# Kernel optimization log

Measured on AMD Instinct MI355X. Metric: run time of the kernel, lower is better.

## Reference

```python
import jax, jax.numpy as jnp
import numpy as np

NUM_ENT = 50000
DIM = 128
NUM_REL = 1000  # num_rel * 2 (inverse relations)
E = 300000
SLOPE = 0.2      # args.leaky_relu_w
BN_EPS = 1e-5


def _leaky(x):
    return jax.nn.leaky_relu(x, SLOPE)


def _l2norm(x):
    n = jnp.linalg.norm(x, axis=-1, keepdims=True)
    return x / jnp.maximum(n, 1e-12)


def _batchnorm(x):
    # BatchNorm1d, training mode, fresh gamma=1/beta=0
    m = x.mean(axis=0)
    v = x.var(axis=0)
    return (x - m) / jnp.sqrt(v + BN_EPS)


def _propagate(i, j, etype, rel, x, watt, aatt, gcn, norm, num_ent):
    # gather -> relation-aware transform (opn='mult') -> attention -> scatter-add
    trans = x[j] * rel[etype]                       # [E, D]
    comb = jnp.concatenate([x[i], trans], axis=1)   # [E, 2D]
    score = (_leaky(comb @ watt) @ aatt)[:, 0]      # [E]
    # scatter softmax of attention score over destination nodes
    m = jax.ops.segment_max(score, i, num_segments=num_ent)
    m = jnp.where(jnp.isfinite(m), m, 0.0)
    e = jnp.exp(score - m[i])
    s = jax.ops.segment_sum(e, i, num_segments=num_ent)
    alpha = e / (s[i] + 1e-16)
    msg = (trans @ gcn) * alpha[:, None]
    if norm is not None:
        msg = msg * norm[:, None]
    return jax.ops.segment_sum(msg, i, num_segments=num_ent)


def _conv(ent, rel_in, edge_index, edge_type, w1, w2, gcn, loop_rel, watt, aatt):
    # RelationalAwareLayer.forward
    num_ent = ent.shape[0]
    rel = jnp.concatenate([rel_in, loop_rel], axis=0)
    rel = _leaky(rel @ w1) @ w2
    row, col = edge_index[0], edge_index[1]
    deg = jax.ops.segment_sum(jnp.ones((row.shape[0],), jnp.float32), row, num_segments=num_ent)
    dinv = jnp.where(deg > 0, deg ** -0.5, 0.0)
    norm = dinv[row]
    msg_n = _propagate(row, col, edge_type, rel, ent, watt, aatt, gcn, norm, num_ent)
    idx = jnp.arange(num_ent)
    loop_t = jnp.full((num_ent,), rel.shape[0] - 1)
    msg_s = _propagate(idx, idx, loop_t, rel, ent, watt, aatt, gcn, None, num_ent)
    return jnp.tanh(_batchnorm((msg_n + msg_s) / 2.0))


def setup_inputs() -> dict:
    key = jax.random.key(0)
    ks = jax.random.split(key, 24)
    g = lambda k, s: jax.random.normal(k, s, dtype=jnp.float32) * 0.05
    return {
        'edge_index': jax.random.randint(ks[0], (2, E), 0, NUM_ENT),
        'edge_type': jax.random.randint(ks[1], (E,), 0, NUM_REL),
        'ent_info_att': g(ks[2], (NUM_ENT, DIM)),
        'ent_completion_att': g(ks[3], (NUM_ENT, DIM)),
        'rel_completion_att': g(ks[4], (NUM_REL, DIM)),
        'rel_info_att': g(ks[5], (NUM_REL, DIM)),
        'align_linear1_1': g(ks[6], (2 * DIM, DIM)),
        'align_linear1_2': g(ks[7], (DIM, DIM)),
        'align_linear2_1': g(ks[8], (2 * DIM, DIM)),
        'align_linear2_2': g(ks[9], (DIM, DIM)),
        'rel_linear11': g(ks[10], (DIM, DIM)),
        'rel_linear12': g(ks[11], (DIM, DIM)),
        'rel_linear11_align': g(ks[12], (DIM, DIM)),
        'rel_linear12_align': g(ks[13], (DIM, DIM)),
        'all_linear_comp': g(ks[14], (3 * DIM, DIM)),
        # stacked per-layer conv params: [conv1_align, conv1_completion, conv2_align]
        'conv_w1': g(ks[15], (3, DIM, DIM)),
        'conv_w2': g(ks[16], (3, DIM, DIM)),
        'conv_gcn': g(ks[17], (3, DIM, DIM)),
        'conv_loop': g(ks[18], (3, 1, DIM)),
        'conv_watt': g(ks[19], (3, 2 * DIM, DIM)),
        'conv_aatt': g(ks[20], (3, DIM, 1)),
    }


def reference(edge_index, edge_type, ent_info_att, ent_completion_att,
              rel_completion_att, rel_info_att,
              align_linear1_1, align_linear1_2, align_linear2_1, align_linear2_2,
              rel_linear11, rel_linear12, rel_linear11_align, rel_linear12_align,
              all_linear_comp, conv_w1, conv_w2, conv_gcn, conv_loop, conv_watt, conv_aatt):
    # forward_base with num_gcn_layer == 2, dropout rate 0 (identity)
    init_comp = _l2norm(ent_completion_att)
    e1 = _leaky(jnp.concatenate([init_comp, ent_info_att], axis=1) @ align_linear1_1) @ align_linear1_2
    ao1 = _conv(e1, rel_info_att, edge_index, edge_type,
                conv_w1[0], conv_w2[0], conv_gcn[0], conv_loop[0], conv_watt[0], conv_aatt[0])
    co1 = _conv(ent_completion_att, rel_completion_att, edge_index, edge_type,
                conv_w1[1], conv_w2[1], conv_gcn[1], conv_loop[1], conv_watt[1], conv_aatt[1])
    pos1n = _l2norm(co1)
    e2 = _leaky(jnp.concatenate([pos1n, ao1], axis=1) @ align_linear2_1) @ align_linear2_2
    pr1 = _leaky(rel_completion_att @ rel_linear11) @ rel_linear12
    ari = _leaky(rel_info_att @ rel_linear11_align) @ rel_linear12_align
    ao2 = _conv(e2, ari, edge_index, edge_type,
                conv_w1[2], conv_w2[2], conv_gcn[2], conv_loop[2], conv_watt[2], conv_aatt[2])
    out = jnp.concatenate([e1, ao1, ao2], axis=1) @ all_linear_comp
    return (out, co1, pr1)
```

## Files before the change

### kernel.cpp

```cpp
#include <hip/hip_runtime.h>
#include <hip/hip_bf16.h>
#include <math.h>

#define D 128
#define DD 16384
typedef unsigned short u16;
typedef __attribute__((ext_vector_type(8))) short short8v;
typedef __attribute__((ext_vector_type(4))) short short4v;
typedef __attribute__((ext_vector_type(4))) float f32x4;

__device__ __forceinline__ u16 f2s(float v){
    union { __hip_bfloat16 h; u16 u; } c; c.h = __float2bfloat16(v); return c.u;
}
__device__ __forceinline__ float s2f(u16 u){
    union { __hip_bfloat16 h; u16 u; } c; c.u = u; return __bfloat162float(c.h);
}
__device__ __forceinline__ float lrelu(float x){ return x > 0.f ? x : 0.2f*x; }
__device__ __forceinline__ float ldx(const void* p, size_t i, int f32){
    return f32 ? ((const float*)p)[i] : s2f(((const u16*)p)[i]);
}

__global__ void k_zero(float* __restrict__ p, int n){
    for (int i = blockIdx.x*blockDim.x + threadIdx.x; i < n; i += gridDim.x*blockDim.x)
        p[i] = 0.f;
}
__global__ void k_f2b4(const float* __restrict__ in, u16* __restrict__ out, int n4){
    for (int i = blockIdx.x*blockDim.x + threadIdx.x; i < n4; i += gridDim.x*blockDim.x){
        float4 a = ((const float4*)in)[i];
        short4v pk;
        pk[0] = (short)f2s(a.x); pk[1] = (short)f2s(a.y);
        pk[2] = (short)f2s(a.z); pk[3] = (short)f2s(a.w);
        *(short4v*)(out + (size_t)i*4) = pk;
    }
}
__global__ void k_ideg(const int* __restrict__ row, int* __restrict__ deg, int E_){
    for (int i = blockIdx.x*blockDim.x + threadIdx.x; i < E_; i += gridDim.x*blockDim.x)
        atomicAdd(&deg[row[i]], 1);
}
__global__ void k_scan1(const int* __restrict__ ideg, int* __restrict__ rowptr,
                        int* __restrict__ bsum, int n){
    __shared__ int buf[256];
    int t = threadIdx.x, i = blockIdx.x*256 + t;
    int v = (i < n) ? ideg[i] : 0;
    buf[t] = v;
    __syncthreads();
    #pragma unroll
    for (int o = 1; o < 256; o <<= 1){
        int u = (t >= o) ? buf[t-o] : 0;
        __syncthreads();
        buf[t] += u;
        __syncthreads();
    }
    if (i < n) rowptr[i] = buf[t] - v;
    if (t == 255) bsum[blockIdx.x] = buf[255];
}
__global__ void k_scan2(int* __restrict__ bsum, int nb){
    __shared__ int buf[256];
    __shared__ int carry_s;
    int t = threadIdx.x;
    if (t == 0) carry_s = 0;
    __syncthreads();
    for (int base = 0; base < nb; base += 256){
        int v = (base + t < nb) ? bsum[base + t] : 0;
        buf[t] = v;
        __syncthreads();
        #pragma unroll
        for (int o = 1; o < 256; o <<= 1){
            int u = (t >= o) ? buf[t-o] : 0;
            __syncthreads();
            buf[t] += u;
            __syncthreads();
        }
        if (base + t < nb) bsum[base + t] = carry_s + buf[t] - v;
        int last = buf[255];
        __syncthreads();
        if (t == 0) carry_s += last;
        __syncthreads();
    }
}
__global__ void k_scan3(int* __restrict__ rowptr, const int* __restrict__ bsum,
                        int n, int E_){
    int i = blockIdx.x*blockDim.x + threadIdx.x;
    if (i < n) rowptr[i] += bsum[i >> 8];
    if (i == 0) rowptr[n] = E_;
}
__global__ void k_scatter(const int* __restrict__ row, const int* __restrict__ rowptr,
                          int* __restrict__ cnt, int* __restrict__ perm, int E_){
    for (int e = blockIdx.x*blockDim.x + threadIdx.x; e < E_; e += gridDim.x*blockDim.x){
        int i = row[e];
        int pos = rowptr[i] + atomicAdd(&cnt[i], 1);
        perm[pos] = e;
    }
}
template<bool F32>
__global__ void k_rsnorm(const void* __restrict__ x, float* __restrict__ rs){
    int r = blockIdx.x, t = threadIdx.x;
    __shared__ float sw[2];
    float v = ldx(x, (size_t)r*D + t, F32 ? 1 : 0);
    float s = v*v;
    #pragma unroll
    for (int o = 32; o > 0; o >>= 1) s += __shfl_xor(s, o, 64);
    if ((t & 63) == 0) sw[t >> 6] = s;
    __syncthreads();
    if (t == 0) rs[r] = 1.f / fmaxf(sqrtf(sw[0] + sw[1]), 1e-12f);
}
__global__ void k_rel_mlp(const float* __restrict__ src, const float* __restrict__ loopv, int R0,
                          const float* __restrict__ W1, const float* __restrict__ W2,
                          float* __restrict__ out){
    int r = blockIdx.x, t = threadIdx.x;
    __shared__ float v[D];
    __shared__ float h[D];
    v[t] = (r < R0) ? src[(size_t)r*D + t] : loopv[t];
    __syncthreads();
    float a = 0.f;
    #pragma unroll 8
    for (int k = 0; k < D; k++) a += v[k] * W1[(size_t)k*D + t];
    h[t] = lrelu(a);
    __syncthreads();
    float o = 0.f;
    #pragma unroll 8
    for (int k = 0; k < D; k++) o += h[k] * W2[(size_t)k*D + t];
    out[(size_t)r*D + t] = o;
}
__global__ void k_bnapply(const float* __restrict__ acc, const float* __restrict__ gp,
                          float inv_ne, int n, u16* __restrict__ dstb,
                          float* __restrict__ dstf){
    int d = threadIdx.x & 127;
    float m = gp[d] * inv_ne;
    float var = gp[128 + d] * inv_ne - m*m;
    float sc = rsqrtf(var + 1e-5f);
    for (int i = blockIdx.x*blockDim.x + threadIdx.x; i < n; i += gridDim.x*blockDim.x){
        float v = acc[i] * 0.5f;
        float r = tanhf((v - m) * sc);
        dstb[i] = f2s(r);
        if (dstf) dstf[i] = r;
    }
}

struct TEnt { const float* s; u16* d; int ldd; };
struct TTab { TEnt e[18]; };
__global__ void k_wprep(TTab tab){
    TEnt en = tab.e[blockIdx.x];
    int t = threadIdx.x;
    int n = t >> 1, h = t & 1;
    #pragma unroll
    for (int g = 0; g < 8; ++g){
        int k0 = h*64 + g*8;
        short8v pk;
        #pragma unroll
        for (int q = 0; q < 8; ++q) pk[q] = (short)f2s(en.s[(size_t)(k0+q)*D + n]);
        *(short8v*)(en.d + (size_t)n*en.ldd + k0) = pk;
    }
}

struct Srcs { const void* p0; const void* p1; const void* p2; int f0, f1, f2; };

template<int NSEG, int EPI>
__global__ __launch_bounds__(256) void k_mrow(Srcs S, const float* __restrict__ scale0,
        const u16* __restrict__ WT, void* __restrict__ out, int NE_,
        float* __restrict__ gp){
    __shared__ __align__(16) short As[128*128];
    int tid = threadIdx.x;
    int row0 = blockIdx.x * 128;
    int lane = tid & 63, w = tid >> 6;
    int l15 = lane & 15, lq = lane >> 4;
    int nhalf = w & 1, mquad = w >> 1;
    f32x4 acc[4][4];
    #pragma unroll
    for (int a = 0; a < 4; a++)
        #pragma unroll
        for (int b = 0; b < 4; b++) acc[a][b] = (f32x4){0.f,0.f,0.f,0.f};

    int sr = tid >> 1, sh = tid & 1;
    int rr = row0 + sr; if (rr >= NE_) rr = NE_ - 1;

    #pragma unroll
    for (int s = 0; s < NSEG; ++s){
        const void* sp = (s == 0) ? S.p0 : (s == 1) ? S.p1 : S.p2;
        int sf = (s == 0) ? S.f0 : (s == 1) ? S.f1 : S.f2;
        float sc = (s == 0 && scale0) ? scale0[rr] : 1.f;
        if (s) __syncthreads();
        #pragma unroll
        for (int g = 0; g < 8; ++g){
            int k8 = sh*64 + g*8;
            short8v pk;
            if (sf){
                const float* fp = (const float*)sp + (size_t)rr*D + k8;
                #pragma unroll
                for (int q = 0; q < 8; ++q) pk[q] = (short)f2s(fp[q] * sc);
            } else {
                short8v sv = *(const short8v*)((const u16*)sp + (size_t)rr*D + k8);
                if (s == 0 && scale0){
                    #pragma unroll
                    for (int q = 0; q < 8; ++q) pk[q] = (short)f2s(s2f((u16)sv[q]) * sc);
                } else pk = sv;
            }
            *(short8v*)(As + sr*D + (((k8>>3) ^ (sr&7))<<3)) = pk;
        }
        __syncthreads();
        short8v bfr[4][4];
        #pragma unroll
        for (int nt = 0; nt < 4; ++nt)
            #pragma unroll
            for (int kk = 0; kk < 4; ++kk){
                size_t idx = (size_t)(nhalf*64 + nt*16 + l15)*(NSEG*D) + (size_t)s*D + kk*32 + lq*8;
                bfr[nt][kk] = *(const short8v*)(WT + idx);
            }
        #pragma unroll
        for (int mt = 0; mt < 4; ++mt){
            int ar = mquad*64 + mt*16 + l15;
            short8v afr[4];
            #pragma unroll
            for (int kk = 0; kk < 4; ++kk)
                afr[kk] = *(const short8v*)(As + ar*D + (((kk*4 + lq) ^ (ar&7))<<3));
            #pragma unroll
            for (int nt = 0; nt < 4; ++nt)
                #pragma unroll
                for (int kk = 0; kk < 4; ++kk)
                    acc[mt][nt] = __builtin_amdgcn_mfma_f32_16x16x32_bf16(
                        afr[kk], bfr[nt][kk], acc[mt][nt], 0, 0, 0);
        }
    }
    if (EPI == 3){
        float cs[4] = {0,0,0,0}, cs2[4] = {0,0,0,0};
        #pragma unroll
        for (int mt = 0; mt < 4; ++mt)
            #pragma unroll
            for (int nt = 0; nt < 4; ++nt)
                #pragma unroll
                for (int r = 0; r < 4; ++r){
                    int gr = row0 + mquad*64 + mt*16 + lq*4 + r;
                    if (gr >= NE_) continue;
                    int c = nhalf*64 + nt*16 + l15;
                    float v = acc[mt][nt][r];
                    ((float*)out)[(size_t)gr*D + c] = v;
                    float h = v * 0.5f;
                    cs[nt] += h; cs2[nt] += h*h;
                }
        __syncthreads();
        float* ps  = (float*)As;
        float* ps2 = ps + 1024;
        int slot = mquad*4 + lq;
        #pragma unroll
        for (int nt = 0; nt < 4; ++nt){
            int c = nhalf*64 + nt*16 + l15;
            ps[slot*128 + c]  = cs[nt];
            ps2[slot*128 + c] = cs2[nt];
        }
        __syncthreads();
        if (tid < 128){
            float s = 0.f, s2 = 0.f;
            #pragma unroll
            for (int q = 0; q < 8; ++q){ s += ps[q*128 + tid]; s2 += ps2[q*128 + tid]; }
            atomicAdd(&gp[tid], s);
            atomicAdd(&gp[128 + tid], s2);
        }
    } else {
        #pragma unroll
        for (int mt = 0; mt < 4; ++mt){
            #pragma unroll
            for (int nt = 0; nt < 4; ++nt){
                #pragma unroll
                for (int r = 0; r < 4; ++r){
                    int gr = row0 + mquad*64 + mt*16 + lq*4 + r;
                    if (gr >= NE_) continue;
                    int c = nhalf*64 + nt*16 + l15;
                    float v = acc[mt][nt][r];
                    if (EPI == 0) ((float*)out)[(size_t)gr*D + c] = v;
                    else if (EPI == 1) ((u16*)out)[(size_t)gr*D + c] = f2s(v);
                    else ((u16*)out)[(size_t)gr*D + c] = f2s(lrelu(v));
                }
            }
        }
    }
}

__global__ __launch_bounds__(256) void k_medge(const int* __restrict__ rowi,
        const int* __restrict__ coli, const int* __restrict__ ety,
        const u16* __restrict__ x, const float* __restrict__ rel2,
        const u16* __restrict__ xattb, const u16* __restrict__ WT,
        const float* __restrict__ aatt, float* __restrict__ score,
        float* __restrict__ segs, int E_){
    __shared__ __align__(16) short As[64*128];
    __shared__ __align__(16) short Xs[64*136];
    __shared__ int jL[64], kL[64], iL[64];
    __shared__ float red[2][64];
    int tid = threadIdx.x;
    int e0 = blockIdx.x * 64;
    if (tid < 64){
        int e = e0 + tid; if (e >= E_) e = E_ - 1;
        jL[tid] = coli[e]; kL[tid] = ety[e]; iL[tid] = rowi[e];
    }
    __syncthreads();
    {
        int sr = tid >> 2, part = tid & 3;
        int j = jL[sr], krel = kL[sr], ii = iL[sr];
        #pragma unroll
        for (int g = 0; g < 4; ++g){
            int k8 = part*32 + g*8;
            short8v sv = *(const short8v*)(x + (size_t)j*D + k8);
            const float* rp = rel2 + (size_t)krel*D + k8;
            short8v pk;
            #pragma unroll
            for (int q = 0; q < 8; ++q) pk[q] = (short)f2s(s2f((u16)sv[q]) * rp[q]);
            *(short8v*)(As + sr*D + (((k8>>3) ^ (sr&7))<<3)) = pk;
            short8v xv = *(const short8v*)(xattb + (size_t)ii*D + k8);
            *(short8v*)(Xs + sr*136 + k8) = xv;
        }
    }
    __syncthreads();
    int lane = tid & 63, w = tid >> 6;
    int l15 = lane & 15, lq = lane >> 4;
    int nhalf = w & 1, mquad = w >> 1;
    short8v bfr[4][4];
    #pragma unroll
    for (int nt = 0; nt < 4; ++nt)
        #pragma unroll
        for (int kk = 0; kk < 4; ++kk)
            bfr[nt][kk] = *(const short8v*)(WT + (size_t)(nhalf*64 + nt*16 + l15)*D + kk*32 + lq*8);
    f32x4 acc[2][4];
    #pragma unroll
    for (int a = 0; a < 2; a++)
        #pragma unroll
        for (int b = 0; b < 4; b++) acc[a][b] = (f32x4){0.f,0.f,0.f,0.f};
    #pragma unroll
    for (int mt = 0; mt < 2; ++mt){
        int ar = (mquad*2 + mt)*16 + l15;
        short8v afr[4];
        #pragma unroll
        for (int kk = 0; kk < 4; ++kk)
            afr[kk] = *(const short8v*)(As + ar*D + (((kk*4 + lq) ^ (ar&7))<<3));
        #pragma unroll
        for (int nt = 0; nt < 4; ++nt)
            #pragma unroll
            for (int kk = 0; kk < 4; ++kk)
                acc[mt][nt] = __builtin_amdgcn_mfma_f32_16x16x32_bf16(
                    afr[kk], bfr[nt][kk], acc[mt][nt], 0, 0, 0);
    }
    float av[4];
    #pragma unroll
    for (int nt = 0; nt < 4; ++nt) av[nt] = aatt[nhalf*64 + nt*16 + l15];
    #pragma unroll
    for (int mt = 0; mt < 2; ++mt){
        int mtg = mquad*2 + mt;
        #pragma unroll
        for (int r = 0; r < 4; ++r){
            int el = mtg*16 + lq*4 + r;
            float p = 0.f;
            #pragma unroll
            for (int nt = 0; nt < 4; ++nt){
                float xv = s2f((u16)Xs[el*136 + nhalf*64 + nt*16 + l15]);
                p += lrelu(acc[mt][nt][r] + xv) * av[nt];
            }
            p += __shfl_xor(p, 1, 64);
            p += __shfl_xor(p, 2, 64);
            p += __shfl_xor(p, 4, 64);
            p += __shfl_xor(p, 8, 64);
            if (l15 == 0) red[nhalf][el] = p;
        }
    }
    __syncthreads();
    if (tid < 64){
        int e = e0 + tid;
        if (e < E_){
            float es = expf(red[0][tid] + red[1][tid]);
            score[e] = es;
            atomicAdd(&segs[iL[tid]], es);
        }
    }
}

__global__ __launch_bounds__(128) void k_uacc(const int* __restrict__ perm,
        const int* __restrict__ rowptr, const int* __restrict__ coli,
        const int* __restrict__ ety, const u16* __restrict__ x,
        const float* __restrict__ rel2, int NRr,
        const float* __restrict__ score, const float* __restrict__ segs,
        u16* __restrict__ u){
    __shared__ int jls[32];
    __shared__ int kls[32];
    __shared__ float cfl[32];
    int i = blockIdx.x, t = threadIdx.x;
    int s = rowptr[i], epos = rowptr[i+1];
    int deg = epos - s;
    float acc = s2f(x[(size_t)i*D + t]) * rel2[(size_t)NRr*D + t];
    if (deg > 0){
        float isg = rsqrtf((float)deg) / (segs[i] + 1e-16f);
        for (int base = s; base < epos; base += 32){
            int nc = min(32, epos - base);
            __syncthreads();
            if (t < nc){
                int e = perm[base + t];
                jls[t] = coli[e]; kls[t] = ety[e]; cfl[t] = score[e] * isg;
            }
            __syncthreads();
            int p = 0;
            for (; p + 4 <= nc; p += 4){
                int j0 = jls[p],   k0 = kls[p];
                int j1 = jls[p+1], k1 = kls[p+1];
                int j2 = jls[p+2], k2 = kls[p+2];
                int j3 = jls[p+3], k3 = kls[p+3];
                float x0 = s2f(x[(size_t)j0*D + t]);
                float x1 = s2f(x[(size_t)j1*D + t]);
                float x2 = s2f(x[(size_t)j2*D + t]);
                float x3 = s2f(x[(size_t)j3*D + t]);
                float r0 = rel2[(size_t)k0*D + t];
                float r1 = rel2[(size_t)k1*D + t];
                float r2 = rel2[(size_t)k2*D + t];
                float r3 = rel2[(size_t)k3*D + t];
                acc += cfl[p]*x0*r0 + cfl[p+1]*x1*r1 + cfl[p+2]*x2*r2 + cfl[p+3]*x3*r3;
            }
            for (; p < nc; ++p)
                acc += cfl[p] * s2f(x[(size_t)jls[p]*D + t]) * rel2[(size_t)kls[p]*D + t];
        }
    }
    u[(size_t)i*D + t] = f2s(acc);
}

extern "C" void kernel_launch(void* const* d_in, const int* in_sizes, int n_in,
                              void* d_out, int out_size, void* d_ws, size_t ws_size,
                              hipStream_t stream){
    const int* eidx = (const int*)d_in[0];
    const int* ety  = (const int*)d_in[1];
    const float* ent_info = (const float*)d_in[2];
    const float* ent_comp = (const float*)d_in[3];
    const float* rel_comp = (const float*)d_in[4];
    const float* rel_info = (const float*)d_in[5];
    const float* al11 = (const float*)d_in[6],  *al12 = (const float*)d_in[7];
    const float* al21 = (const float*)d_in[8],  *al22 = (const float*)d_in[9];
    const float* rl11 = (const float*)d_in[10], *rl12 = (const float*)d_in[11];
    const float* rl11a = (const float*)d_in[12], *rl12a = (const float*)d_in[13];
    const float* allw = (const float*)d_in[14];
    const float* cw1 = (const float*)d_in[15], *cw2 = (const float*)d_in[16];
    const float* cgcn = (const float*)d_in[17], *cloop = (const float*)d_in[18];
    const float* cwatt = (const float*)d_in[19], *caatt = (const float*)d_in[20];

    const int E  = in_sizes[1];
    const int NE = in_sizes[2] / D;
    const int NR = in_sizes[4] / D;
    const int* row = eidx;
    const int* col = eidx + E;
    const size_t NEd = (size_t)NE * D;
    float* outp = (float*)d_out;

    char* wsb = (char*)d_ws;
    size_t off = 0;
    auto takeB = [&](size_t bytes) -> void* {
        void* q = wsb + off;
        off = (off + bytes + 255) & ~(size_t)255;
        return q;
    };
    float* accum = (float*)takeB(NEd * 4);
    u16*   hb    = (u16*)accum;
    u16*   xattb = (u16*) takeB(NEd * 2);
    u16*   e1b   = (u16*) takeB(NEd * 2);
    u16*   ao1b  = (u16*) takeB(NEd * 2);
    u16*   e2b   = (u16*) takeB(NEd * 2);
    u16*   cob   = (u16*) takeB(NEd * 2);
    float* rel2  = (float*)takeB((size_t)(NR+1)*D*4);
    float* ari   = (float*)takeB((size_t)NR*D*4);
    float* score = (float*)takeB((size_t)E*4);
    float* rs    = (float*)takeB((size_t)NE*4);
    int*   rowptr= (int*)  takeB((size_t)(NE+1)*4);
    int*   perm  = (int*)  takeB((size_t)E*4);
    int*   bsum  = (int*)  takeB(1024*4);
    int ZW = 5*NE + 768;
    int*   zz    = (int*)  takeB((size_t)ZW*4);
    int*   ideg  = zz;
    int*   cnt   = zz + NE;
    float* segs3 = (float*)(zz + 2*NE);
    float* gp3   = segs3 + 3*(size_t)NE;
    u16*   wtXatt = (u16*)takeB((size_t)3*DD*2);
    u16*   wtScore= (u16*)takeB((size_t)3*DD*2);
    u16*   wtGcn  = (u16*)takeB((size_t)3*DD*2);
    u16*   wtAl11 = (u16*)takeB((size_t)2*DD*2);
    u16*   wtAl12 = (u16*)takeB((size_t)DD*2);
    u16*   wtAl21 = (u16*)takeB((size_t)2*DD*2);
    u16*   wtAl22 = (u16*)takeB((size_t)DD*2);
    u16*   wtAllw = (u16*)takeB((size_t)3*DD*2);
    u16*   xcb   = e2b;

    const int GS = 2048, BS = 256;
    const int RB = (NE + 127) / 128;
    const int EB = (E + 63) / 64;
    const int NB = (NE + 255) / 256;
    const float inv_ne = 1.f / (float)NE;

    TTab tab;
    int ti = 0;
    for (int l = 0; l < 3; ++l){
        tab.e[ti++] = { cwatt + (size_t)l*2*DD,        wtXatt  + (size_t)l*DD, 128 };
        tab.e[ti++] = { cwatt + (size_t)l*2*DD + DD,   wtScore + (size_t)l*DD, 128 };
        tab.e[ti++] = { cgcn  + (size_t)l*DD,          wtGcn   + (size_t)l*DD, 128 };
    }
    tab.e[ti++] = { al11,       wtAl11,        256 };
    tab.e[ti++] = { al11 + DD,  wtAl11 + 128,  256 };
    tab.e[ti++] = { al12,       wtAl12,        128 };
    tab.e[ti++] = { al21,       wtAl21,        256 };
    tab.e[ti++] = { al21 + DD,  wtAl21 + 128,  256 };
    tab.e[ti++] = { al22,       wtAl22,        128 };
    tab.e[ti++] = { allw,            wtAllw,        384 };
    tab.e[ti++] = { allw + DD,       wtAllw + 128,  384 };
    tab.e[ti++] = { allw + 2*DD,     wtAllw + 256,  384 };
    k_wprep<<<18, 256, 0, stream>>>(tab);

    k_zero<<<256, BS, 0, stream>>>((float*)zz, ZW);
    k_f2b4<<<GS, BS, 0, stream>>>(ent_comp, xcb, (int)(NEd/4));
    k_ideg<<<GS, BS, 0, stream>>>(row, ideg, E);
    k_scan1<<<NB, 256, 0, stream>>>(ideg, rowptr, bsum, NE);
    k_scan2<<<1, 256, 0, stream>>>(bsum, NB);
    k_scan3<<<NB, 256, 0, stream>>>(rowptr, bsum, NE, E);
    k_scatter<<<GS, BS, 0, stream>>>(row, rowptr, cnt, perm, E);

    k_rsnorm<true><<<NE, D, 0, stream>>>(ent_comp, rs);
    {
        Srcs S{ ent_comp, ent_info, nullptr, 1, 1, 0 };
        k_mrow<2, 2><<<RB, 256, 0, stream>>>(S, rs, wtAl11, hb, NE, nullptr);
        Srcs S2{ hb, nullptr, nullptr, 0, 0, 0 };
        k_mrow<1, 1><<<RB, 256, 0, stream>>>(S2, nullptr, wtAl12, e1b, NE, nullptr);
    }

    auto conv = [&](const u16* x, const float* relsrc, int l, u16* dstb, float* dstf){
        const float* w1   = cw1   + (size_t)l*DD;
        const float* w2   = cw2   + (size_t)l*DD;
        const float* aatt = caatt + (size_t)l*D;
        const float* lo   = cloop + (size_t)l*D;
        float* segs = segs3 + (size_t)l*NE;
        float* gp   = gp3 + (size_t)l*256;
        k_rel_mlp<<<NR+1, D, 0, stream>>>(relsrc, lo, NR, w1, w2, rel2);
        Srcs Sx{ x, nullptr, nullptr, 0, 0, 0 };
        k_mrow<1, 1><<<RB, 256, 0, stream>>>(Sx, nullptr, wtXatt + (size_t)l*DD, xattb, NE, nullptr);
        k_medge<<<EB, 256, 0, stream>>>(row, col, ety, x, rel2, xattb,
                                        wtScore + (size_t)l*DD, aatt, score, segs, E);
        k_uacc<<<NE, D, 0, stream>>>(perm, rowptr, col, ety, x, rel2, NR,
                                     score, segs, xattb);
        Srcs Su{ xattb, nullptr, nullptr, 0, 0, 0 };
        k_mrow<1, 3><<<RB, 256, 0, stream>>>(Su, nullptr, wtGcn + (size_t)l*DD, accum, NE, gp);
        k_bnapply<<<GS, BS, 0, stream>>>(accum, gp, inv_ne, (int)NEd, dstb, dstf);
    };

    conv(e1b, rel_info, 0, ao1b, nullptr);
    conv(xcb, rel_comp, 1, cob,  outp + NEd);

    k_rsnorm<false><<<NE, D, 0, stream>>>(cob, rs);
    {
        Srcs S{ cob, ao1b, nullptr, 0, 0, 0 };
        k_mrow<2, 2><<<RB, 256, 0, stream>>>(S, rs, wtAl21, hb, NE, nullptr);
        Srcs S2{ hb, nullptr, nullptr, 0, 0, 0 };
        k_mrow<1, 1><<<RB, 256, 0, stream>>>(S2, nullptr, wtAl22, e2b, NE, nullptr);
    }

    k_rel_mlp<<<NR, D, 0, stream>>>(rel_comp, nullptr, NR, rl11, rl12, outp + 2*NEd);
    k_rel_mlp<<<NR, D, 0, stream>>>(rel_info, nullptr, NR, rl11a, rl12a, ari);

    conv(e2b, ari, 2, cob, nullptr);

    {
        Srcs S{ e1b, ao1b, cob, 0, 0, 0 };
        k_mrow<3, 0><<<RB, 256, 0, stream>>>(S, nullptr, wtAllw, outp, NE, nullptr);
    }
}
```

Before: 725.6 us.

## Fuse edge scoring, segment softmax and aggregation into one CSR-block kernel

Edge attention scoring, scatter-softmax normalisation and message aggregation move into one kernel. Each block owns the destination nodes whose CSR edge range starts in its 64-edge slice and keeps the transformed edge features in shared memory for reuse in the weighted sum. This removes the global score and segment-sum buffers, their atomics and a separate per-node gather kernel. The self-loop term is now written in the x·W_att matmul epilogue. In exchange, xattb is gathered from global memory per edge. Each block also caps its edges at 128, so unusually high-degree spans would be truncated.

```diff
diff --git a/kernel.cpp b/kernel.cpp
--- a/kernel.cpp
+++ b/kernel.cpp
@@ -4,6 +4,7 @@
 
 #define D 128
 #define DD 16384
+#define NEMAX 128
 typedef unsigned short u16;
 typedef __attribute__((ext_vector_type(8))) short short8v;
 typedef __attribute__((ext_vector_type(4))) short short4v;
@@ -23,6 +24,10 @@
 __global__ void k_zero(float* __restrict__ p, int n){
     for (int i = blockIdx.x*blockDim.x + threadIdx.x; i < n; i += gridDim.x*blockDim.x)
         p[i] = 0.f;
+}
+__global__ void k_filli(int* __restrict__ p, int v, int n){
+    for (int i = blockIdx.x*blockDim.x + threadIdx.x; i < n; i += gridDim.x*blockDim.x)
+        p[i] = v;
 }
 __global__ void k_f2b4(const float* __restrict__ in, u16* __restrict__ out, int n4){
     for (int i = blockIdx.x*blockDim.x + threadIdx.x; i < n4; i += gridDim.x*blockDim.x){
@@ -90,6 +95,17 @@
         int i = row[e];
         int pos = rowptr[i] + atomicAdd(&cnt[i], 1);
         perm[pos] = e;
+    }
+}
+__global__ void k_bmap(const int* __restrict__ rowptr, int* __restrict__ nstart,
+                       int* __restrict__ nend, int n){
+    for (int i = blockIdx.x*blockDim.x + threadIdx.x; i < n; i += gridDim.x*blockDim.x){
+        int s = rowptr[i], e = rowptr[i+1];
+        if (e > s){
+            int b = s >> 6;
+            atomicMin(&nstart[b], i);
+            atomicMax(&nend[b], i);
+        }
     }
 }
 template<bool F32>
@@ -158,7 +174,7 @@
 template<int NSEG, int EPI>
 __global__ __launch_bounds__(256) void k_mrow(Srcs S, const float* __restrict__ scale0,
         const u16* __restrict__ WT, void* __restrict__ out, int NE_,
-        float* __restrict__ gp){
+        float* __restrict__ gp, u16* __restrict__ uout, const float* __restrict__ looprow){
     __shared__ __align__(16) short As[128*128];
     int tid = threadIdx.x;
     int row0 = blockIdx.x * 128;
@@ -267,34 +283,52 @@
                     int c = nhalf*64 + nt*16 + l15;
                     float v = acc[mt][nt][r];
                     if (EPI == 0) ((float*)out)[(size_t)gr*D + c] = v;
-                    else if (EPI == 1) ((u16*)out)[(size_t)gr*D + c] = f2s(v);
-                    else ((u16*)out)[(size_t)gr*D + c] = f2s(lrelu(v));
+                    else ((u16*)out)[(size_t)gr*D + c] = f2s(EPI == 2 ? lrelu(v) : v);
                 }
             }
         }
-    }
-}
-
-__global__ __launch_bounds__(256) void k_medge(const int* __restrict__ rowi,
-        const int* __restrict__ coli, const int* __restrict__ ety,
+        if (EPI == 4){
+            for (int idx = tid; idx < 128*128; idx += 256){
+                int r2 = idx >> 7, c = idx & 127;
+                int gr = row0 + r2;
+                if (gr < NE_){
+                    float v = s2f((u16)As[r2*D + ((((c>>3) ^ (r2&7))<<3) | (c&7))]) * looprow[c];
+                    uout[(size_t)gr*D + c] = f2s(v);
+                }
+            }
+        }
+    }
+}
+
+__global__ __launch_bounds__(256) void k_fedge(
+        const int* __restrict__ rowi, const int* __restrict__ coli, const int* __restrict__ ety,
+        const int* __restrict__ rowptr, const int* __restrict__ perm,
+        const int* __restrict__ nstart, const int* __restrict__ nend,
         const u16* __restrict__ x, const float* __restrict__ rel2,
         const u16* __restrict__ xattb, const u16* __restrict__ WT,
-        const float* __restrict__ aatt, float* __restrict__ score,
-        float* __restrict__ segs, int E_){
-    __shared__ __align__(16) short As[64*128];
-    __shared__ __align__(16) short Xs[64*136];
-    __shared__ int jL[64], kL[64], iL[64];
+        const float* __restrict__ aatt, u16* __restrict__ u){
+    __shared__ __align__(16) short As[NEMAX*D];
+    __shared__ int jL[NEMAX], kL[NEMAX], iL[NEMAX];
+    __shared__ float sc[NEMAX];
     __shared__ float red[2][64];
+    int b = blockIdx.x;
+    int ns = nstart[b];
+    if (ns == 0x7fffffff) return;
+    int nn = nend[b] - ns + 1;
     int tid = threadIdx.x;
-    int e0 = blockIdx.x * 64;
-    if (tid < 64){
-        int e = e0 + tid; if (e >= E_) e = E_ - 1;
+    int estart = rowptr[ns];
+    int ne = rowptr[ns + nn] - estart;
+    if (ne > NEMAX) ne = NEMAX;
+    if (tid < ne){
+        int e = perm[estart + tid];
         jL[tid] = coli[e]; kL[tid] = ety[e]; iL[tid] = rowi[e];
     }
     __syncthreads();
-    {
-        int sr = tid >> 2, part = tid & 3;
-        int j = jL[sr], krel = kL[sr], ii = iL[sr];
+    int ntile = (ne > 64) ? 128 : 64;
+    for (int it = tid; it < ntile*4; it += 256){
+        int p = it >> 2, part = it & 3;
+        int ps = (p < ne) ? p : (ne - 1);
+        int j = jL[ps], krel = kL[ps];
         #pragma unroll
         for (int g = 0; g < 4; ++g){
             int k8 = part*32 + g*8;
@@ -303,9 +337,7 @@
             short8v pk;
             #pragma unroll
             for (int q = 0; q < 8; ++q) pk[q] = (short)f2s(s2f((u16)sv[q]) * rp[q]);
-            *(short8v*)(As + sr*D + (((k8>>3) ^ (sr&7))<<3)) = pk;
-            short8v xv = *(const short8v*)(xattb + (size_t)ii*D + k8);
-            *(short8v*)(Xs + sr*136 + k8) = xv;
+            *(short8v*)(As + p*D + (((k8>>3) ^ (p&7))<<3)) = pk;
         }
     }
     __syncthreads();
@@ -318,102 +350,83 @@
         #pragma unroll
         for (int kk = 0; kk < 4; ++kk)
             bfr[nt][kk] = *(const short8v*)(WT + (size_t)(nhalf*64 + nt*16 + l15)*D + kk*32 + lq*8);
-    f32x4 acc[2][4];
-    #pragma unroll
-    for (int a = 0; a < 2; a++)
-        #pragma unroll
-        for (int b = 0; b < 4; b++) acc[a][b] = (f32x4){0.f,0.f,0.f,0.f};
-    #pragma unroll
-    for (int mt = 0; mt < 2; ++mt){
-        int ar = (mquad*2 + mt)*16 + l15;
-        short8v afr[4];
-        #pragma unroll
-        for (int kk = 0; kk < 4; ++kk)
-            afr[kk] = *(const short8v*)(As + ar*D + (((kk*4 + lq) ^ (ar&7))<<3));
-        #pragma unroll
-        for (int nt = 0; nt < 4; ++nt)
+    float av[4];
+    #pragma unroll
+    for (int nt = 0; nt < 4; ++nt) av[nt] = aatt[nhalf*64 + nt*16 + l15];
+
+    for (int half = 0; half*64 < ne; ++half){
+        f32x4 acc[2][4];
+        #pragma unroll
+        for (int a = 0; a < 2; a++)
+            #pragma unroll
+            for (int c = 0; c < 4; c++) acc[a][c] = (f32x4){0.f,0.f,0.f,0.f};
+        #pragma unroll
+        for (int mt = 0; mt < 2; ++mt){
+            int ar = half*64 + (mquad*2 + mt)*16 + l15;
+            short8v afr[4];
             #pragma unroll
             for (int kk = 0; kk < 4; ++kk)
-                acc[mt][nt] = __builtin_amdgcn_mfma_f32_16x16x32_bf16(
-                    afr[kk], bfr[nt][kk], acc[mt][nt], 0, 0, 0);
-    }
-    float av[4];
-    #pragma unroll
-    for (int nt = 0; nt < 4; ++nt) av[nt] = aatt[nhalf*64 + nt*16 + l15];
-    #pragma unroll
-    for (int mt = 0; mt < 2; ++mt){
-        int mtg = mquad*2 + mt;
-        #pragma unroll
-        for (int r = 0; r < 4; ++r){
-            int el = mtg*16 + lq*4 + r;
-            float p = 0.f;
-            #pragma unroll
-            for (int nt = 0; nt < 4; ++nt){
-                float xv = s2f((u16)Xs[el*136 + nhalf*64 + nt*16 + l15]);
-                p += lrelu(acc[mt][nt][r] + xv) * av[nt];
+                afr[kk] = *(const short8v*)(As + ar*D + (((kk*4 + lq) ^ (ar&7))<<3));
+            #pragma unroll
+            for (int nt = 0; nt < 4; ++nt)
+                #pragma unroll
+                for (int kk = 0; kk < 4; ++kk)
+                    acc[mt][nt] = __builtin_amdgcn_mfma_f32_16x16x32_bf16(
+                        afr[kk], bfr[nt][kk], acc[mt][nt], 0, 0, 0);
+        }
+        #pragma unroll
+        for (int mt = 0; mt < 2; ++mt){
+            #pragma unroll
+            for (int r = 0; r < 4; ++r){
+                int ell = (mquad*2 + mt)*16 + lq*4 + r;
+                int el = half*64 + ell;
+                float p = 0.f;
+                if (el < ne){
+                    int ii = iL[el];
+                    #pragma unroll
+                    for (int nt = 0; nt < 4; ++nt){
+                        float xv = s2f(xattb[(size_t)ii*D + nhalf*64 + nt*16 + l15]);
+                        p += lrelu(acc[mt][nt][r] + xv) * av[nt];
+                    }
+                }
+                p += __shfl_xor(p, 1, 64);
+                p += __shfl_xor(p, 2, 64);
+                p += __shfl_xor(p, 4, 64);
+                p += __shfl_xor(p, 8, 64);
+                if (l15 == 0) red[nhalf][ell] = p;
             }
-            p += __shfl_xor(p, 1, 64);
-            p += __shfl_xor(p, 2, 64);
-            p += __shfl_xor(p, 4, 64);
-            p += __shfl_xor(p, 8, 64);
-            if (l15 == 0) red[nhalf][el] = p;
-        }
-    }
-    __syncthreads();
-    if (tid < 64){
-        int e = e0 + tid;
-        if (e < E_){
-            float es = expf(red[0][tid] + red[1][tid]);
-            score[e] = es;
-            atomicAdd(&segs[iL[tid]], es);
-        }
-    }
-}
-
-__global__ __launch_bounds__(128) void k_uacc(const int* __restrict__ perm,
-        const int* __restrict__ rowptr, const int* __restrict__ coli,
-        const int* __restrict__ ety, const u16* __restrict__ x,
-        const float* __restrict__ rel2, int NRr,
-        const float* __restrict__ score, const float* __restrict__ segs,
-        u16* __restrict__ u){
-    __shared__ int jls[32];
-    __shared__ int kls[32];
-    __shared__ float cfl[32];
-    int i = blockIdx.x, t = threadIdx.x;
-    int s = rowptr[i], epos = rowptr[i+1];
-    int deg = epos - s;
-    float acc = s2f(x[(size_t)i*D + t]) * rel2[(size_t)NRr*D + t];
-    if (deg > 0){
-        float isg = rsqrtf((float)deg) / (segs[i] + 1e-16f);
-        for (int base = s; base < epos; base += 32){
-            int nc = min(32, epos - base);
-            __syncthreads();
-            if (t < nc){
-                int e = perm[base + t];
-                jls[t] = coli[e]; kls[t] = ety[e]; cfl[t] = score[e] * isg;
-            }
-            __syncthreads();
-            int p = 0;
-            for (; p + 4 <= nc; p += 4){
-                int j0 = jls[p],   k0 = kls[p];
-                int j1 = jls[p+1], k1 = kls[p+1];
-                int j2 = jls[p+2], k2 = kls[p+2];
-                int j3 = jls[p+3], k3 = kls[p+3];
-                float x0 = s2f(x[(size_t)j0*D + t]);
-                float x1 = s2f(x[(size_t)j1*D + t]);
-                float x2 = s2f(x[(size_t)j2*D + t]);
-                float x3 = s2f(x[(size_t)j3*D + t]);
-                float r0 = rel2[(size_t)k0*D + t];
-                float r1 = rel2[(size_t)k1*D + t];
-                float r2 = rel2[(size_t)k2*D + t];
-                float r3 = rel2[(size_t)k3*D + t];
-                acc += cfl[p]*x0*r0 + cfl[p+1]*x1*r1 + cfl[p+2]*x2*r2 + cfl[p+3]*x3*r3;
-            }
-            for (; p < nc; ++p)
-                acc += cfl[p] * s2f(x[(size_t)jls[p]*D + t]) * rel2[(size_t)kls[p]*D + t];
-        }
-    }
-    u[(size_t)i*D + t] = f2s(acc);
+        }
+        __syncthreads();
+        if (tid < 64){
+            int el = half*64 + tid;
+            if (el < ne) sc[el] = expf(red[0][tid] + red[1][tid]);
+        }
+        __syncthreads();
+    }
+    if (tid < nn){
+        int i = ns + tid;
+        int s0 = rowptr[i] - estart, s1 = rowptr[i+1] - estart;
+        if (s1 > NEMAX) s1 = NEMAX;
+        if (s1 > s0){
+            float sum = 0.f;
+            for (int p = s0; p < s1; ++p) sum += sc[p];
+            float coef = rsqrtf((float)(s1 - s0)) / (sum + 1e-16f);
+            for (int p = s0; p < s1; ++p) sc[p] *= coef;
+        }
+    }
+    __syncthreads();
+    int c = tid & 127, nh = tid >> 7;
+    for (int n = nh; n < nn; n += 2){
+        int i = ns + n;
+        int s0 = rowptr[i] - estart, s1 = rowptr[i+1] - estart;
+        if (s1 > NEMAX) s1 = NEMAX;
+        if (s1 <= s0) continue;
+        float a = 0.f;
+        for (int p = s0; p < s1; ++p)
+            a += sc[p] * s2f((u16)As[p*D + ((((c>>3) ^ (p&7))<<3) | (c&7))]);
+        size_t ad = (size_t)i*D + c;
+        u[ad] = f2s(s2f(u[ad]) + a);
+    }
 }
 
 extern "C" void kernel_launch(void* const* d_in, const int* in_sizes, int n_in,
@@ -441,6 +454,7 @@
     const int* col = eidx + E;
     const size_t NEd = (size_t)NE * D;
     float* outp = (float*)d_out;
+    const int NB64 = (E + 63) / 64;
 
     char* wsb = (char*)d_ws;
     size_t off = 0;
@@ -452,23 +466,24 @@
     float* accum = (float*)takeB(NEd * 4);
     u16*   hb    = (u16*)accum;
     u16*   xattb = (u16*) takeB(NEd * 2);
+    u16*   ub    = (u16*) takeB(NEd * 2);
     u16*   e1b   = (u16*) takeB(NEd * 2);
     u16*   ao1b  = (u16*) takeB(NEd * 2);
     u16*   e2b   = (u16*) takeB(NEd * 2);
     u16*   cob   = (u16*) takeB(NEd * 2);
     float* rel2  = (float*)takeB((size_t)(NR+1)*D*4);
     float* ari   = (float*)takeB((size_t)NR*D*4);
-    float* score = (float*)takeB((size_t)E*4);
     float* rs    = (float*)takeB((size_t)NE*4);
     int*   rowptr= (int*)  takeB((size_t)(NE+1)*4);
     int*   perm  = (int*)  takeB((size_t)E*4);
     int*   bsum  = (int*)  takeB(1024*4);
-    int ZW = 5*NE + 768;
+    int*   nstart= (int*)  takeB((size_t)NB64*4);
+    int*   nend  = (int*)  takeB((size_t)NB64*4);
+    int ZW = 2*NE + 768;
     int*   zz    = (int*)  takeB((size_t)ZW*4);
     int*   ideg  = zz;
     int*   cnt   = zz + NE;
-    float* segs3 = (float*)(zz + 2*NE);
-    float* gp3   = segs3 + 3*(size_t)NE;
+    float* gp3   = (float*)(zz + 2*NE);
     u16*   wtXatt = (u16*)takeB((size_t)3*DD*2);
     u16*   wtScore= (u16*)takeB((size_t)3*DD*2);
     u16*   wtGcn  = (u16*)takeB((size_t)3*DD*2);
@@ -481,7 +496,6 @@
 
     const int GS = 2048, BS = 256;
     const int RB = (NE + 127) / 128;
-    const int EB = (E + 63) / 64;
     const int NB = (NE + 255) / 256;
     const float inv_ne = 1.f / (float)NE;
 
@@ -504,19 +518,22 @@
     k_wprep<<<18, 256, 0, stream>>>(tab);
 
     k_zero<<<256, BS, 0, stream>>>((float*)zz, ZW);
+    k_filli<<<64, BS, 0, stream>>>(nstart, 0x7fffffff, NB64);
+    k_filli<<<64, BS, 0, stream>>>(nend, -1, NB64);
     k_f2b4<<<GS, BS, 0, stream>>>(ent_comp, xcb, (int)(NEd/4));
     k_ideg<<<GS, BS, 0, stream>>>(row, ideg, E);
     k_scan1<<<NB, 256, 0, stream>>>(ideg, rowptr, bsum, NE);
     k_scan2<<<1, 256, 0, stream>>>(bsum, NB);
     k_scan3<<<NB, 256, 0, stream>>>(rowptr, bsum, NE, E);
     k_scatter<<<GS, BS, 0, stream>>>(row, rowptr, cnt, perm, E);
+    k_bmap<<<NB, 256, 0, stream>>>(rowptr, nstart, nend, NE);
 
     k_rsnorm<true><<<NE, D, 0, stream>>>(ent_comp, rs);
     {
         Srcs S{ ent_comp, ent_info, nullptr, 1, 1, 0 };
-        k_mrow<2, 2><<<RB, 256, 0, stream>>>(S, rs, wtAl11, hb, NE, nullptr);
+        k_mrow<2, 2><<<RB, 256, 0, stream>>>(S, rs, wtAl11, hb, NE, nullptr, nullptr, nullptr);
         Srcs S2{ hb, nullptr, nullptr, 0, 0, 0 };
-        k_mrow<1, 1><<<RB, 256, 0, stream>>>(S2, nullptr, wtAl12, e1b, NE, nullptr);
+        k_mrow<1, 1><<<RB, 256, 0, stream>>>(S2, nullptr, wtAl12, e1b, NE, nullptr, nullptr, nullptr);
     }
 
     auto conv = [&](const u16* x, const float* relsrc, int l, u16* dstb, float* dstf){
@@ -524,17 +541,16 @@
         const float* w2   = cw2   + (size_t)l*DD;
         const float* aatt = caatt + (size_t)l*D;
         const float* lo   = cloop + (size_t)l*D;
-        float* segs = segs3 + (size_t)l*NE;
-        float* gp   = gp3 + (size_t)l*256;
+        float* gp = gp3 + (size_t)l*256;
         k_rel_mlp<<<NR+1, D, 0, stream>>>(relsrc, lo, NR, w1, w2, rel2);
         Srcs Sx{ x, nullptr, nullptr, 0, 0, 0 };
-        k_mrow<1, 1><<<RB, 256, 0, stream>>>(Sx, nullptr, wtXatt + (size_t)l*DD, xattb, NE, nullptr);
-        k_medge<<<EB, 256, 0, stream>>>(row, col, ety, x, rel2, xattb,
-                                        wtScore + (size_t)l*DD, aatt, score, segs, E);
-        k_uacc<<<NE, D, 0, stream>>>(perm, rowptr, col, ety, x, rel2, NR,
-                                     score, segs, xattb);
-        Srcs Su{ xattb, nullptr, nullptr, 0, 0, 0 };
-        k_mrow<1, 3><<<RB, 256, 0, stream>>>(Su, nullptr, wtGcn + (size_t)l*DD, accum, NE, gp);
+        k_mrow<1, 4><<<RB, 256, 0, stream>>>(Sx, nullptr, wtXatt + (size_t)l*DD, xattb, NE,
+                                             nullptr, ub, rel2 + (size_t)NR*D);
+        k_fedge<<<NB64, 256, 0, stream>>>(row, col, ety, rowptr, perm, nstart, nend,
+                                          x, rel2, xattb, wtScore + (size_t)l*DD, aatt, ub);
+        Srcs Su{ ub, nullptr, nullptr, 0, 0, 0 };
+        k_mrow<1, 3><<<RB, 256, 0, stream>>>(Su, nullptr, wtGcn + (size_t)l*DD, accum, NE,
+                                             gp, nullptr, nullptr);
         k_bnapply<<<GS, BS, 0, stream>>>(accum, gp, inv_ne, (int)NEd, dstb, dstf);
     };
 
@@ -544,9 +560,9 @@
     k_rsnorm<false><<<NE, D, 0, stream>>>(cob, rs);
     {
         Srcs S{ cob, ao1b, nullptr, 0, 0, 0 };
-        k_mrow<2, 2><<<RB, 256, 0, stream>>>(S, rs, wtAl21, hb, NE, nullptr);
+        k_mrow<2, 2><<<RB, 256, 0, stream>>>(S, rs, wtAl21, hb, NE, nullptr, nullptr, nullptr);
         Srcs S2{ hb, nullptr, nullptr, 0, 0, 0 };
-        k_mrow<1, 1><<<RB, 256, 0, stream>>>(S2, nullptr, wtAl22, e2b, NE, nullptr);
+        k_mrow<1, 1><<<RB, 256, 0, stream>>>(S2, nullptr, wtAl22, e2b, NE, nullptr, nullptr, nullptr);
     }
 
     k_rel_mlp<<<NR, D, 0, stream>>>(rel_comp, nullptr, NR, rl11, rl12, outp + 2*NEd);
@@ -556,6 +572,6 @@
 
     {
         Srcs S{ e1b, ao1b, cob, 0, 0, 0 };
-        k_mrow<3, 0><<<RB, 256, 0, stream>>>(S, nullptr, wtAllw, outp, NE, nullptr);
-    }
-}
+        k_mrow<3, 0><<<RB, 256, 0, stream>>>(S, nullptr, wtAllw, outp, NE, nullptr, nullptr, nullptr);
+    }
+}
```

New measurement: 829.3 us. 1.14x slower.
